# Kernel tuning notes

Measured on AMD Instinct MI355X. Metric: run time of the kernel, lower is better.

## Reference

```python
import jax, jax.numpy as jnp
import numpy as np

N_ATOMS = 50000
N_NBRS = 32
R_CUTOFF = 5.0
N_BASIS = 128
N_FILTERS = 128
N_GAUSS = 25
MAX_Z = 100
MEAN = 0.0
STDDEV = 20.0


def ssp(x):
    # shifted softplus: softplus(x) - log(2)
    return jax.nn.softplus(x) - jnp.log(2.0)


def setup_inputs() -> dict:
    key = jax.random.key(0)
    ks = jax.random.split(key, 18)
    dR = jax.random.uniform(ks[0], (N_ATOMS, N_NBRS), dtype=jnp.float32) * R_CUTOFF
    Z = jax.random.randint(ks[1], (N_ATOMS,), 0, MAX_Z)
    nbr_idx = jax.random.randint(ks[2], (N_ATOMS, N_NBRS), 0, N_ATOMS)

    def p(k, shape):
        fan_in = shape[0]
        return (jax.random.normal(k, shape, dtype=jnp.float32) / np.sqrt(fan_in)).astype(jnp.float32)

    return dict(
        dR=dR, Z=Z, nbr_idx=nbr_idx,
        embed_table=jax.random.normal(ks[3], (MAX_Z, N_BASIS), dtype=jnp.float32),
        fw1=p(ks[4], (N_GAUSS, N_FILTERS)), fb1=jnp.zeros((N_FILTERS,), jnp.float32),
        fw2=p(ks[5], (N_FILTERS, N_FILTERS)), fb2=jnp.zeros((N_FILTERS,), jnp.float32),
        in2f_w=p(ks[6], (N_BASIS, N_FILTERS)),
        f2out_w1=p(ks[7], (N_FILTERS, N_BASIS)), f2out_b1=jnp.zeros((N_BASIS,), jnp.float32),
        f2out_w2=p(ks[8], (N_BASIS, N_BASIS)), f2out_b2=jnp.zeros((N_BASIS,), jnp.float32),
        mlp_w1=p(ks[9], (N_BASIS, 64)), mlp_b1=jnp.zeros((64,), jnp.float32),
        mlp_w2=p(ks[10], (64, 1)), mlp_b2=jnp.zeros((1,), jnp.float32),
    )


def reference(dR, Z, nbr_idx, embed_table, fw1, fb1, fw2, fb2, in2f_w,
              f2out_w1, f2out_b1, f2out_w2, f2out_b2,
              mlp_w1, mlp_b1, mlp_w2, mlp_b2):
    # embedding lookup: [N, B]
    x = embed_table[Z]

    # gaussian smearing of distances: [N, K, G]
    offsets = jnp.linspace(0.0, R_CUTOFF, N_GAUSS, dtype=jnp.float32)
    coeff = -0.5 / (offsets[1] - offsets[0]) ** 2
    dr_exp = jnp.exp(coeff * (dR[..., None] - offsets) ** 2)

    # filter network: Dense+ssp, Dense -> [N, K, F]
    W = ssp(jnp.einsum('nkg,gf->nkf', dr_exp, fw1) + fb1)
    W = jnp.einsum('nkf,fh->nkh', W, fw2) + fb2

    # cosine cutoff
    fcut = 0.5 * (jnp.cos(dR * jnp.pi / R_CUTOFF) + 1.0) * (dR < R_CUTOFF)
    W = W * fcut[..., None]

    # cfconv: in2f (no bias), neighbor gather, elementwise filter, sum over neighbors
    y = x @ in2f_w                    # [N, F]
    y_nbrs = y[nbr_idx]               # [N, K, F] irregular gather
    mask = (nbr_idx < N_ATOMS)[..., None]
    agg = jnp.sum(jnp.where(mask, y_nbrs * W, 0.0), axis=1)  # [N, F]

    # f2out: Dense+ssp, Dense
    v = ssp(agg @ f2out_w1 + f2out_b1) @ f2out_w2 + f2out_b2

    # residual update
    x = x + v

    # atomwise MLP [128 -> 64 -> 1] with ssp between layers
    yi = ssp(x @ mlp_w1 + mlp_b1) @ mlp_w2 + mlp_b2  # [N, 1]
    yi = yi * STDDEV + MEAN

    # aggregate (sum over atom axis), per_atom=False
    return jnp.sum(yi, axis=0)  # [1]
```

## Files before the change

kernel.cpp:

```cpp
#include <hip/hip_runtime.h>
#include <math.h>

#define N_ATOMS  50000
#define N_NBRS   32
#define N_GAUSS  25
#define RCUT     5.0f
#define TT       192
#define TROWS    32
#define NTB      6
#define MAXZ     100
#define NT32     1563
#define PBLOCKS  256
#define PI_F     3.14159265358979323846f

typedef unsigned int   uint_t;
typedef unsigned short ushort_t;
typedef _Float16 f16;
typedef f16   f16x2 __attribute__((ext_vector_type(2)));
typedef f16   f16x4 __attribute__((ext_vector_type(4)));
typedef f16   f16x8 __attribute__((ext_vector_type(8)));
typedef float f32x4 __attribute__((ext_vector_type(4)));

__device__ __forceinline__ float ssp(float x) {
  return fmaxf(x, 0.0f) + __logf(fmaf(0.5f, __expf(-fabsf(x)), 0.5f));
}
__device__ __forceinline__ f16x2 bch(uint_t u) {
  return __builtin_bit_cast(f16x2, u);
}
__device__ __forceinline__ uint_t hcb(f16x2 v) {
  return __builtin_bit_cast(uint_t, v);
}
__device__ __forceinline__ int swz(int m, int e) {
  return m * 128 + ((((e >> 3) ^ m) & 15) << 3) + (e & 7);
}

__global__ void __launch_bounds__(256, 2)
prep_all_kernel(const float* __restrict__ fw1,
                const float* __restrict__ fb1,
                const float* __restrict__ fw2,
                const float* __restrict__ fb2,
                const float* __restrict__ w1,
                const float* __restrict__ w2,
                const float* __restrict__ mw1,
                const float* __restrict__ embed,
                const float* __restrict__ in2f,
                f16* __restrict__ tabh,
                f16* __restrict__ ytab,
                f16* __restrict__ w1ht,
                f16* __restrict__ w2ht,
                f16* __restrict__ mw1ht) {
  const int tid = threadIdx.x;
  const int bid = blockIdx.x;

  __shared__ float sW2[128 * 128];
  __shared__ float sH[TROWS][128];

  if (bid < NTB) {
    const int i0 = bid * TROWS;
    #pragma unroll
    for (int t = 0; t < 16; ++t) {
      const int e = tid + t * 256;
      ((float4*)sW2)[e] = ((const float4*)fw2)[e];
    }
    {
      const int f  = tid & 127;
      const int rh = (tid >> 7) * (TROWS / 2);
      const float delta = RCUT / (float)(N_GAUSS - 1);
      const float coeff = -0.5f / (delta * delta);
      const float b1v = fb1[f];
      for (int j = 0; j < TROWS / 2; ++j) {
        const float r = (float)(i0 + rh + j) * (RCUT / 191.0f);
        float h = b1v;
        #pragma unroll
        for (int g = 0; g < N_GAUSS; ++g) {
          const float d = r - (float)g * delta;
          h = fmaf(__expf(coeff * d * d), fw1[g * 128 + f], h);
        }
        sH[rh + j][f] = ssp(h);
      }
    }
    __syncthreads();
    {
      const int c0 = (tid & 31) * 4;
      const int rg = (tid >> 5) * 4;
      f32x4 acc[4];
      const float4 bv = *(const float4*)&fb2[c0];
      #pragma unroll
      for (int j = 0; j < 4; ++j) acc[j] = (f32x4){bv.x, bv.y, bv.z, bv.w};
      for (int k = 0; k < 128; ++k) {
        const float4 wv = *(const float4*)&sW2[k * 128 + c0];
        #pragma unroll
        for (int j = 0; j < 4; ++j) {
          const float hv = sH[rg + j][k];
          acc[j][0] = fmaf(hv, wv.x, acc[j][0]);
          acc[j][1] = fmaf(hv, wv.y, acc[j][1]);
          acc[j][2] = fmaf(hv, wv.z, acc[j][2]);
          acc[j][3] = fmaf(hv, wv.w, acc[j][3]);
        }
      }
      #pragma unroll
      for (int j = 0; j < 4; ++j) {
        const int i = i0 + rg + j;
        const float r = (float)i * (RCUT / 191.0f);
        const float fc = (r < RCUT) ? 0.5f * (__cosf(r * PI_F / RCUT) + 1.0f) : 0.0f;
        f16x4 o;
        #pragma unroll
        for (int c = 0; c < 4; ++c) o[c] = (f16)(acc[j][c] * fc);
        *(f16x4*)&tabh[i * 128 + c0] = o;
      }
    }
  } else {
    const int cc = (bid - NTB) * 2 + (tid >> 7);
    const int i  = tid & 127;
    w1ht[cc * 128 + i] = (f16)w1[i * 128 + cc];
    w2ht[cc * 128 + i] = (f16)w2[i * 128 + cc];
    if (cc < 64) mw1ht[cc * 128 + i] = (f16)mw1[i * 64 + cc];
    float* xs = &sH[0][0] + (tid >> 7) * 128;
    xs[i] = (cc < MAXZ) ? embed[cc * 128 + i] : 0.0f;
    __syncthreads();
    if (cc < MAXZ) {
      float acc = 0.0f;
      for (int j = 0; j < 128; j += 4) {
        const float4 xv = *reinterpret_cast<const float4*>(&xs[j]);
        acc = fmaf(xv.x, in2f[(j + 0) * 128 + i], acc);
        acc = fmaf(xv.y, in2f[(j + 1) * 128 + i], acc);
        acc = fmaf(xv.z, in2f[(j + 2) * 128 + i], acc);
        acc = fmaf(xv.w, in2f[(j + 3) * 128 + i], acc);
      }
      ytab[cc * 128 + i] = (f16)acc;
    }
  }
}

__global__ void __launch_bounds__(512, 2)
fused_kernel(const float* __restrict__ dR,
             const int* __restrict__ Z,
             const int* __restrict__ nbr,
             const float* __restrict__ embed,
             const f16* __restrict__ tabh,
             const f16* __restrict__ ytab,
             const f16* __restrict__ w1ht, const float* __restrict__ b1,
             const f16* __restrict__ w2ht, const float* __restrict__ b2,
             const f16* __restrict__ mw1ht, const float* __restrict__ mb1,
             const float* __restrict__ mw2,
             float* __restrict__ partial) {
  const int tid = threadIdx.x;
  const int w   = tid >> 6;
  const int l   = tid & 63;
  const int q   = l >> 4;
  const int cq  = l & 15;
  __shared__ __align__(16) f16    sW[TT * 128];
  __shared__ __align__(16) f16    sYT[MAXZ * 128];
  __shared__ __align__(16) uint_t s_pk[1024];
  __shared__ __align__(16) f16    sA[2][16 * 128];
  __shared__ __align__(16) f16    sB[2][16 * 128];
  __shared__ int   sZ[32];
  __shared__ float sRed[8];

  for (int e = tid; e < TT * 16; e += 512)   ((uint4*)sW)[e]  = ((const uint4*)tabh)[e];
  for (int e = tid; e < MAXZ * 16; e += 512) ((uint4*)sYT)[e] = ((const uint4*)ytab)[e];

  const int g   = w >> 2;
  const int wvg = w & 3;
  const int rc  = cq;
  const int qk  = q;
  f16x8 bw1[2][4], bw2[2][4], bwm[4];
  float bb1[2], bb2[2];
  #pragma unroll
  for (int t = 0; t < 2; ++t) {
    const int c = wvg * 32 + t * 16 + rc;
    bb1[t] = b1[c];
    bb2[t] = b2[c];
    #pragma unroll
    for (int k0i = 0; k0i < 4; ++k0i) {
      bw1[t][k0i] = *(const f16x8*)&w1ht[c * 128 + k0i * 32 + qk * 8];
      bw2[t][k0i] = *(const f16x8*)&w2ht[c * 128 + k0i * 32 + qk * 8];
    }
  }
  const int c1 = wvg * 16 + rc;
  #pragma unroll
  for (int k0i = 0; k0i < 4; ++k0i) {
    bwm[k0i] = *(const f16x8*)&mw1ht[c1 * 128 + k0i * 32 + qk * 8];
  }
  const float bm = mb1[c1];
  const float cm = mw2[c1];

  const int m = w * 4 + q;
  const char* wb = (const char*)sW  + cq * 16;
  const char* yb = (const char*)sYT + cq * 16;

  float vsum = 0.0f;
  __syncthreads();

#define AFRAG(SRC, k0) (*(const f16x8*)&SRC[rc * 128 + (((((k0) >> 3) + qk) ^ rc) & 15) * 8])

  for (int chunk = blockIdx.x; chunk < NT32; chunk += PBLOCKS) {
    const int a0 = chunk * 32;
    __syncthreads();

    #pragma unroll
    for (int t0 = 0; t0 < 2; ++t0) {
      const int t = tid + t0 * 512;
      const int pidx = a0 * N_NBRS + t;
      uint_t pk = 0;
      if (pidx < N_ATOMS * N_NBRS) {
        const float r = dR[pidx];
        const int  nb = nbr[pidx];
        int i0 = (int)(r * (191.0f / RCUT) + 0.5f);
        i0 = min(i0, 191);
        pk = (uint_t)i0 | ((uint_t)Z[nb] << 8);
      }
      s_pk[t] = pk;
    }
    if (tid < 32) sZ[tid] = (a0 + tid < N_ATOMS) ? Z[a0 + tid] : 0;
    __syncthreads();

    {
      f16x2 acc[4];
      #pragma unroll
      for (int c = 0; c < 4; ++c) acc[c] = (f16x2)0;

      uint4 twA[4], ytA[4], twB[4], ytB[4];

#define IG(BK, gi) { \
    _Pragma("unroll") \
    for (int d = 0; d < 4; ++d) { \
      const uint_t pk = s_pk[m * N_NBRS + (gi) * 4 + d]; \
      tw##BK[d] = *(const uint4*)(wb + ((pk & 0xFFu) << 8)); \
      yt##BK[d] = *(const uint4*)(yb + ((pk >> 8) << 8)); \
    } }

#define CG(BK) { \
    _Pragma("unroll") \
    for (int d = 0; d < 4; ++d) { \
      acc[0] += bch(tw##BK[d].x) * bch(yt##BK[d].x); \
      acc[1] += bch(tw##BK[d].y) * bch(yt##BK[d].y); \
      acc[2] += bch(tw##BK[d].z) * bch(yt##BK[d].z); \
      acc[3] += bch(tw##BK[d].w) * bch(yt##BK[d].w); \
    } }

      IG(A, 0) IG(B, 1)
      CG(A) IG(A, 2)
      CG(B) IG(B, 3)
      CG(A) IG(A, 4)
      CG(B) IG(B, 5)
      CG(A) IG(A, 6)
      CG(B) IG(B, 7)
      CG(A)
      CG(B)
#undef IG
#undef CG

      uint4 o;
      o.x = hcb(acc[0]); o.y = hcb(acc[1]); o.z = hcb(acc[2]); o.w = hcb(acc[3]);
      const int mm = m & 15;
      *(uint4*)&sA[m >> 4][mm * 128 + (((cq ^ mm) & 15) << 3)] = o;
    }
    __syncthreads();

    f32x4 dacc[2];
    #pragma unroll
    for (int t = 0; t < 2; ++t) dacc[t] = (f32x4){bb1[t], bb1[t], bb1[t], bb1[t]};
    #pragma unroll
    for (int k0i = 0; k0i < 4; ++k0i) {
      const f16x8 af = AFRAG(sA[g], k0i * 32);
      #pragma unroll
      for (int t = 0; t < 2; ++t)
        dacc[t] = __builtin_amdgcn_mfma_f32_16x16x32_f16(af, bw1[t][k0i], dacc[t], 0, 0, 0);
    }
    #pragma unroll
    for (int t = 0; t < 2; ++t) {
      const int c = wvg * 32 + t * 16 + rc;
      #pragma unroll
      for (int r = 0; r < 4; ++r) sB[g][swz(qk * 4 + r, c)] = (f16)ssp(dacc[t][r]);
    }
    __syncthreads();

    #pragma unroll
    for (int t = 0; t < 2; ++t) dacc[t] = (f32x4){bb2[t], bb2[t], bb2[t], bb2[t]};
    #pragma unroll
    for (int k0i = 0; k0i < 4; ++k0i) {
      const f16x8 af = AFRAG(sB[g], k0i * 32);
      #pragma unroll
      for (int t = 0; t < 2; ++t)
        dacc[t] = __builtin_amdgcn_mfma_f32_16x16x32_f16(af, bw2[t][k0i], dacc[t], 0, 0, 0);
    }
    #pragma unroll
    for (int t = 0; t < 2; ++t) {
      const int c = wvg * 32 + t * 16 + rc;
      #pragma unroll
      for (int r = 0; r < 4; ++r) {
        const int mm = qk * 4 + r;
        const float x = embed[(size_t)sZ[g * 16 + mm] * 128 + c] + dacc[t][r];
        sA[g][swz(mm, c)] = (f16)x;
      }
    }
    __syncthreads();

    f32x4 a2 = (f32x4){bm, bm, bm, bm};
    #pragma unroll
    for (int k0i = 0; k0i < 4; ++k0i)
      a2 = __builtin_amdgcn_mfma_f32_16x16x32_f16(AFRAG(sA[g], k0i * 32), bwm[k0i], a2, 0, 0, 0);
    #pragma unroll
    for (int r = 0; r < 4; ++r) {
      const int atom = a0 + g * 16 + qk * 4 + r;
      if (atom < N_ATOMS) vsum = fmaf(ssp(a2[r]), cm, vsum);
    }
  }
#undef AFRAG

  #pragma unroll
  for (int o = 1; o < 64; o <<= 1) vsum += __shfl_xor(vsum, o, 64);
  if (l == 0) sRed[w] = vsum;
  __syncthreads();
  if (tid == 0) {
    float s = 0.0f;
    #pragma unroll
    for (int i = 0; i < 8; ++i) s += sRed[i];
    partial[blockIdx.x] = s;
  }
}

__global__ void __launch_bounds__(256, 1)
reduce_kernel(const float* __restrict__ partial,
              const float* __restrict__ mb2,
              float* __restrict__ out) {
  const int tid = threadIdx.x;
  float s = (tid < PBLOCKS) ? partial[tid] : 0.0f;
  __shared__ float sr[4];
  #pragma unroll
  for (int o = 1; o < 64; o <<= 1) s += __shfl_xor(s, o, 64);
  if ((tid & 63) == 0) sr[tid >> 6] = s;
  __syncthreads();
  if (tid == 0) {
    out[0] = 20.0f * (sr[0] + sr[1] + sr[2] + sr[3] + (float)N_ATOMS * mb2[0]);
  }
}

extern "C" void kernel_launch(void* const* d_in, const int* in_sizes, int n_in,
                              void* d_out, int out_size, void* d_ws, size_t ws_size,
                              hipStream_t stream) {
  const float* dR    = (const float*)d_in[0];
  const int*   Z     = (const int*)  d_in[1];
  const int*   nbr   = (const int*)  d_in[2];
  const float* embed = (const float*)d_in[3];
  const float* fw1   = (const float*)d_in[4];
  const float* fb1   = (const float*)d_in[5];
  const float* fw2   = (const float*)d_in[6];
  const float* fb2   = (const float*)d_in[7];
  const float* in2f  = (const float*)d_in[8];
  const float* w1    = (const float*)d_in[9];
  const float* b1    = (const float*)d_in[10];
  const float* w2    = (const float*)d_in[11];
  const float* b2    = (const float*)d_in[12];
  const float* mw1   = (const float*)d_in[13];
  const float* mb1   = (const float*)d_in[14];
  const float* mw2   = (const float*)d_in[15];
  const float* mb2   = (const float*)d_in[16];
  float* out = (float*)d_out;

  char* ws = (char*)d_ws;
  f16*   tabh    = (f16*)ws;
  f16*   ytab    = (f16*)(ws + (size_t)64 * 1024);
  f16*   w1ht    = (f16*)(ws + (size_t)128 * 1024);
  f16*   w2ht    = (f16*)(ws + (size_t)192 * 1024);
  f16*   mw1ht   = (f16*)(ws + (size_t)256 * 1024);
  float* partial = (float*)(ws + (size_t)384 * 1024);

  prep_all_kernel<<<NTB + 64, 256, 0, stream>>>(fw1, fb1, fw2, fb2,
      w1, w2, mw1, embed, in2f, tabh, ytab, w1ht, w2ht, mw1ht);
  fused_kernel<<<PBLOCKS, 512, 0, stream>>>(dR, Z, nbr, embed,
      tabh, ytab, w1ht, b1, w2ht, b2, mw1ht, mb1, mw2, partial);
  reduce_kernel<<<1, 256, 0, stream>>>(partial, mb2, out);
}
```

Baseline: 55.64 us.

## Warp-specialize fused kernel into gather producer and MFMA consumer waves

The block grows to 1024 threads. Waves 0-7 do the neighbor gather and aggregation for chunk s into a double-buffered shared aggregate, while waves 8-15 run the dense MLP chain on chunk s-1. This overlaps the LDS gather phase with the matrix-core phase, which the old kernel ran serially. In exchange the kernel uses more shared memory and more barriers per stage, and launch_bounds(1024,4) limits registers per thread and may cause spilling. It also risks lower occupancy.

```diff
diff --git a/kernel.cpp b/kernel.cpp
--- a/kernel.cpp
+++ b/kernel.cpp
@@ -132,7 +132,7 @@
   }
 }
 
-__global__ void __launch_bounds__(512, 2)
+__global__ void __launch_bounds__(1024, 4)
 fused_kernel(const float* __restrict__ dR,
              const int* __restrict__ Z,
              const int* __restrict__ nbr,
@@ -144,88 +144,70 @@
              const f16* __restrict__ mw1ht, const float* __restrict__ mb1,
              const float* __restrict__ mw2,
              float* __restrict__ partial) {
-  const int tid = threadIdx.x;
-  const int w   = tid >> 6;
-  const int l   = tid & 63;
-  const int q   = l >> 4;
-  const int cq  = l & 15;
+  const int tid  = threadIdx.x;
+  const int wave = tid >> 6;
+  const int l    = tid & 63;
+  const int q    = l >> 4;
+  const int cq   = l & 15;
+  const int bid  = blockIdx.x;
+
   __shared__ __align__(16) f16    sW[TT * 128];
   __shared__ __align__(16) f16    sYT[MAXZ * 128];
-  __shared__ __align__(16) uint_t s_pk[1024];
-  __shared__ __align__(16) f16    sA[2][16 * 128];
-  __shared__ __align__(16) f16    sB[2][16 * 128];
-  __shared__ int   sZ[32];
+  __shared__ __align__(16) uint_t s_pk[2][1024];
+  __shared__ __align__(16) f16    aggB[2][32 * 128];
+  __shared__ __align__(16) f16    sB[32 * 128];
+  __shared__ __align__(16) f16    sX[32 * 128];
+  __shared__ int   sZb[2][32];
   __shared__ float sRed[8];
 
-  for (int e = tid; e < TT * 16; e += 512)   ((uint4*)sW)[e]  = ((const uint4*)tabh)[e];
-  for (int e = tid; e < MAXZ * 16; e += 512) ((uint4*)sYT)[e] = ((const uint4*)ytab)[e];
-
-  const int g   = w >> 2;
-  const int wvg = w & 3;
-  const int rc  = cq;
-  const int qk  = q;
-  f16x8 bw1[2][4], bw2[2][4], bwm[4];
-  float bb1[2], bb2[2];
-  #pragma unroll
-  for (int t = 0; t < 2; ++t) {
-    const int c = wvg * 32 + t * 16 + rc;
-    bb1[t] = b1[c];
-    bb2[t] = b2[c];
-    #pragma unroll
-    for (int k0i = 0; k0i < 4; ++k0i) {
-      bw1[t][k0i] = *(const f16x8*)&w1ht[c * 128 + k0i * 32 + qk * 8];
-      bw2[t][k0i] = *(const f16x8*)&w2ht[c * 128 + k0i * 32 + qk * 8];
-    }
-  }
-  const int c1 = wvg * 16 + rc;
-  #pragma unroll
-  for (int k0i = 0; k0i < 4; ++k0i) {
-    bwm[k0i] = *(const f16x8*)&mw1ht[c1 * 128 + k0i * 32 + qk * 8];
-  }
-  const float bm = mb1[c1];
-  const float cm = mw2[c1];
-
-  const int m = w * 4 + q;
-  const char* wb = (const char*)sW  + cq * 16;
-  const char* yb = (const char*)sYT + cq * 16;
-
-  float vsum = 0.0f;
+  for (int e = tid; e < TT * 16; e += 1024)   ((uint4*)sW)[e]  = ((const uint4*)tabh)[e];
+  for (int e = tid; e < MAXZ * 16; e += 1024) ((uint4*)sYT)[e] = ((const uint4*)ytab)[e];
   __syncthreads();
 
-#define AFRAG(SRC, k0) (*(const f16x8*)&SRC[rc * 128 + (((((k0) >> 3) + qk) ^ rc) & 15) * 8])
-
-  for (int chunk = blockIdx.x; chunk < NT32; chunk += PBLOCKS) {
-    const int a0 = chunk * 32;
-    __syncthreads();
-
-    #pragma unroll
-    for (int t0 = 0; t0 < 2; ++t0) {
-      const int t = tid + t0 * 512;
-      const int pidx = a0 * N_NBRS + t;
-      uint_t pk = 0;
-      if (pidx < N_ATOMS * N_NBRS) {
-        const float r = dR[pidx];
-        const int  nb = nbr[pidx];
-        int i0 = (int)(r * (191.0f / RCUT) + 0.5f);
-        i0 = min(i0, 191);
-        pk = (uint_t)i0 | ((uint_t)Z[nb] << 8);
-      }
-      s_pk[t] = pk;
-    }
-    if (tid < 32) sZ[tid] = (a0 + tid < N_ATOMS) ? Z[a0 + tid] : 0;
-    __syncthreads();
-
-    {
+  const int myChunks = (NT32 - 1 - bid) / PBLOCKS + 1;
+  const int nstages  = myChunks + 1;
+
+#define AFRAGP(P, k0) (*(const f16x8*)&(P)[rc * 128 + (((((k0) >> 3) + qk) ^ rc) & 15) * 8])
+
+  if (wave < 8) {
+    const int m = wave * 4 + q;
+    const char* wb = (const char*)sW  + cq * 16;
+    const char* yb = (const char*)sYT + cq * 16;
+
+    for (int s = 0; s < nstages; ++s) {
+      const int c   = bid + s * PBLOCKS;
+      const bool act = (c < NT32);
+      const int b   = s & 1;
+      const int a0  = c * 32;
+
+      if (act) {
+        #pragma unroll
+        for (int t0 = 0; t0 < 2; ++t0) {
+          const int t = tid + t0 * 512;
+          const int pidx = a0 * N_NBRS + t;
+          uint_t pk = 0;
+          if (pidx < N_ATOMS * N_NBRS) {
+            const float r = dR[pidx];
+            const int  nb = nbr[pidx];
+            int i0 = (int)(r * (191.0f / RCUT) + 0.5f);
+            i0 = min(i0, 191);
+            pk = (uint_t)i0 | ((uint_t)Z[nb] << 8);
+          }
+          s_pk[b][t] = pk;
+        }
+        if (tid < 32) sZb[b][tid] = (a0 + tid < N_ATOMS) ? Z[a0 + tid] : 0;
+      }
+      __syncthreads();
+
       f16x2 acc[4];
       #pragma unroll
-      for (int c = 0; c < 4; ++c) acc[c] = (f16x2)0;
-
+      for (int cch = 0; cch < 4; ++cch) acc[cch] = (f16x2)0;
       uint4 twA[4], ytA[4], twB[4], ytB[4];
 
 #define IG(BK, gi) { \
     _Pragma("unroll") \
     for (int d = 0; d < 4; ++d) { \
-      const uint_t pk = s_pk[m * N_NBRS + (gi) * 4 + d]; \
+      const uint_t pk = s_pk[b][m * N_NBRS + (gi) * 4 + d]; \
       tw##BK[d] = *(const uint4*)(wb + ((pk & 0xFFu) << 8)); \
       yt##BK[d] = *(const uint4*)(yb + ((pk >> 8) << 8)); \
     } }
@@ -239,85 +221,136 @@
       acc[3] += bch(tw##BK[d].w) * bch(yt##BK[d].w); \
     } }
 
-      IG(A, 0) IG(B, 1)
-      CG(A) IG(A, 2)
-      CG(B) IG(B, 3)
-      CG(A) IG(A, 4)
-      CG(B) IG(B, 5)
-      CG(A) IG(A, 6)
-      CG(B) IG(B, 7)
-      CG(A)
-      CG(B)
+      if (act) {
+        IG(A, 0) IG(B, 1)
+        CG(A) IG(A, 2)
+        CG(B) IG(B, 3)
+        CG(A)
+        CG(B)
+      }
+      __syncthreads();
+
+      if (act) {
+        IG(A, 4) IG(B, 5)
+        CG(A) IG(A, 6)
+        CG(B) IG(B, 7)
+        CG(A)
+        CG(B)
+        uint4 o;
+        o.x = hcb(acc[0]); o.y = hcb(acc[1]); o.z = hcb(acc[2]); o.w = hcb(acc[3]);
+        const int mm = m & 15;
+        *(uint4*)&aggB[b][(m >> 4) * 2048 + mm * 128 + (((cq ^ mm) & 15) << 3)] = o;
+      }
+      __syncthreads();
 #undef IG
 #undef CG
-
-      uint4 o;
-      o.x = hcb(acc[0]); o.y = hcb(acc[1]); o.z = hcb(acc[2]); o.w = hcb(acc[3]);
-      const int mm = m & 15;
-      *(uint4*)&sA[m >> 4][mm * 128 + (((cq ^ mm) & 15) << 3)] = o;
-    }
-    __syncthreads();
-
-    f32x4 dacc[2];
-    #pragma unroll
-    for (int t = 0; t < 2; ++t) dacc[t] = (f32x4){bb1[t], bb1[t], bb1[t], bb1[t]};
-    #pragma unroll
-    for (int k0i = 0; k0i < 4; ++k0i) {
-      const f16x8 af = AFRAG(sA[g], k0i * 32);
-      #pragma unroll
-      for (int t = 0; t < 2; ++t)
-        dacc[t] = __builtin_amdgcn_mfma_f32_16x16x32_f16(af, bw1[t][k0i], dacc[t], 0, 0, 0);
-    }
+    }
+  } else {
+    const int cw  = wave - 8;
+    const int g   = cw >> 2;
+    const int wvg = cw & 3;
+    const int rc  = cq;
+    const int qk  = q;
+
+    f16x8 bw1[2][4], bw2[2][4], bwm[4];
+    float bb1[2], bb2[2];
     #pragma unroll
     for (int t = 0; t < 2; ++t) {
       const int c = wvg * 32 + t * 16 + rc;
+      bb1[t] = b1[c];
+      bb2[t] = b2[c];
       #pragma unroll
-      for (int r = 0; r < 4; ++r) sB[g][swz(qk * 4 + r, c)] = (f16)ssp(dacc[t][r]);
-    }
-    __syncthreads();
-
-    #pragma unroll
-    for (int t = 0; t < 2; ++t) dacc[t] = (f32x4){bb2[t], bb2[t], bb2[t], bb2[t]};
-    #pragma unroll
-    for (int k0i = 0; k0i < 4; ++k0i) {
-      const f16x8 af = AFRAG(sB[g], k0i * 32);
-      #pragma unroll
-      for (int t = 0; t < 2; ++t)
-        dacc[t] = __builtin_amdgcn_mfma_f32_16x16x32_f16(af, bw2[t][k0i], dacc[t], 0, 0, 0);
-    }
-    #pragma unroll
-    for (int t = 0; t < 2; ++t) {
-      const int c = wvg * 32 + t * 16 + rc;
-      #pragma unroll
-      for (int r = 0; r < 4; ++r) {
-        const int mm = qk * 4 + r;
-        const float x = embed[(size_t)sZ[g * 16 + mm] * 128 + c] + dacc[t][r];
-        sA[g][swz(mm, c)] = (f16)x;
-      }
-    }
-    __syncthreads();
-
-    f32x4 a2 = (f32x4){bm, bm, bm, bm};
+      for (int k0i = 0; k0i < 4; ++k0i) {
+        bw1[t][k0i] = *(const f16x8*)&w1ht[c * 128 + k0i * 32 + qk * 8];
+        bw2[t][k0i] = *(const f16x8*)&w2ht[c * 128 + k0i * 32 + qk * 8];
+      }
+    }
+    const int c1 = wvg * 16 + rc;
     #pragma unroll
     for (int k0i = 0; k0i < 4; ++k0i)
-      a2 = __builtin_amdgcn_mfma_f32_16x16x32_f16(AFRAG(sA[g], k0i * 32), bwm[k0i], a2, 0, 0, 0);
+      bwm[k0i] = *(const f16x8*)&mw1ht[c1 * 128 + k0i * 32 + qk * 8];
+    const float bm = mb1[c1];
+    const float cm = mw2[c1];
+
+    float vsum = 0.0f;
+
+    for (int s = 0; s < nstages; ++s) {
+      const int cc  = bid + (s - 1) * PBLOCKS;
+      const bool act = (s >= 1) && (cc < NT32);
+      const int bb  = (s - 1) & 1;
+      const f16* agg = &aggB[bb][g * 2048];
+      f16* hB = &sB[g * 2048];
+      f16* hX = &sX[g * 2048];
+
+      f32x4 dacc[2];
+      if (act) {
+        #pragma unroll
+        for (int t = 0; t < 2; ++t) dacc[t] = (f32x4){bb1[t], bb1[t], bb1[t], bb1[t]};
+        #pragma unroll
+        for (int k0i = 0; k0i < 4; ++k0i) {
+          const f16x8 af = AFRAGP(agg, k0i * 32);
+          #pragma unroll
+          for (int t = 0; t < 2; ++t)
+            dacc[t] = __builtin_amdgcn_mfma_f32_16x16x32_f16(af, bw1[t][k0i], dacc[t], 0, 0, 0);
+        }
+        #pragma unroll
+        for (int t = 0; t < 2; ++t) {
+          const int c = wvg * 32 + t * 16 + rc;
+          #pragma unroll
+          for (int r = 0; r < 4; ++r) hB[swz(qk * 4 + r, c)] = (f16)ssp(dacc[t][r]);
+        }
+      }
+      __syncthreads();
+
+      if (act) {
+        #pragma unroll
+        for (int t = 0; t < 2; ++t) dacc[t] = (f32x4){bb2[t], bb2[t], bb2[t], bb2[t]};
+        #pragma unroll
+        for (int k0i = 0; k0i < 4; ++k0i) {
+          const f16x8 af = AFRAGP(hB, k0i * 32);
+          #pragma unroll
+          for (int t = 0; t < 2; ++t)
+            dacc[t] = __builtin_amdgcn_mfma_f32_16x16x32_f16(af, bw2[t][k0i], dacc[t], 0, 0, 0);
+        }
+        #pragma unroll
+        for (int t = 0; t < 2; ++t) {
+          const int c = wvg * 32 + t * 16 + rc;
+          #pragma unroll
+          for (int r = 0; r < 4; ++r) {
+            const int mm = qk * 4 + r;
+            const float x = embed[(size_t)sZb[bb][g * 16 + mm] * 128 + c] + dacc[t][r];
+            hX[swz(mm, c)] = (f16)x;
+          }
+        }
+      }
+      __syncthreads();
+
+      if (act) {
+        f32x4 a2 = (f32x4){bm, bm, bm, bm};
+        #pragma unroll
+        for (int k0i = 0; k0i < 4; ++k0i)
+          a2 = __builtin_amdgcn_mfma_f32_16x16x32_f16(AFRAGP(hX, k0i * 32), bwm[k0i], a2, 0, 0, 0);
+        #pragma unroll
+        for (int r = 0; r < 4; ++r) {
+          const int atom = cc * 32 + g * 16 + qk * 4 + r;
+          if (atom < N_ATOMS) vsum = fmaf(ssp(a2[r]), cm, vsum);
+        }
+      }
+      __syncthreads();
+    }
+
     #pragma unroll
-    for (int r = 0; r < 4; ++r) {
-      const int atom = a0 + g * 16 + qk * 4 + r;
-      if (atom < N_ATOMS) vsum = fmaf(ssp(a2[r]), cm, vsum);
-    }
+    for (int o = 1; o < 64; o <<= 1) vsum += __shfl_xor(vsum, o, 64);
+    if (l == 0) sRed[cw] = vsum;
   }
-#undef AFRAG
-
-  #pragma unroll
-  for (int o = 1; o < 64; o <<= 1) vsum += __shfl_xor(vsum, o, 64);
-  if (l == 0) sRed[w] = vsum;
+#undef AFRAGP
+
   __syncthreads();
   if (tid == 0) {
-    float s = 0.0f;
+    float sF = 0.0f;
     #pragma unroll
-    for (int i = 0; i < 8; ++i) s += sRed[i];
-    partial[blockIdx.x] = s;
+    for (int i = 0; i < 8; ++i) sF += sRed[i];
+    partial[bid] = sF;
   }
 }
 
@@ -326,7 +359,8 @@
               const float* __restrict__ mb2,
               float* __restrict__ out) {
   const int tid = threadIdx.x;
-  float s = (tid < PBLOCKS) ? partial[tid] : 0.0f;
+  float s = 0.0f;
+  for (int i = tid; i < PBLOCKS; i += 256) s += partial[i];
   __shared__ float sr[4];
   #pragma unroll
   for (int o = 1; o < 64; o <<= 1) s += __shfl_xor(s, o, 64);
@@ -369,7 +403,7 @@
 
   prep_all_kernel<<<NTB + 64, 256, 0, stream>>>(fw1, fb1, fw2, fb2,
       w1, w2, mw1, embed, in2f, tabh, ytab, w1ht, w2ht, mw1ht);
-  fused_kernel<<<PBLOCKS, 512, 0, stream>>>(dR, Z, nbr, embed,
+  fused_kernel<<<PBLOCKS, 1024, 0, stream>>>(dR, Z, nbr, embed,
       tabh, ytab, w1ht, b1, w2ht, b2, mw1ht, mb1, mw2, partial);
   reduce_kernel<<<1, 256, 0, stream>>>(partial, mb2, out);
 }
```

Result: slower. 57.78 us (+3.9%).

## Software-pipeline neighbor gather of next chunk with MFMA dense stages of current

Applied to the files above, without the earlier changes.

Restructures the per-chunk loop into a two-stage software pipeline. The packed neighbor indices and the LDS gather-accumulate for chunk s+1 are interleaved with the three MFMA dense stages of chunk s, using double-buffered s_pk, aggregate and Z buffers. The aim is to hide LDS gather latency and global load latency behind matrix work and cut idle time at barriers. In exchange it needs more LDS (extra double buffers) and more live registers, which may lower occupancy below two blocks per CU.

```diff
diff --git a/kernel.cpp b/kernel.cpp
--- a/kernel.cpp
+++ b/kernel.cpp
@@ -149,12 +149,15 @@
   const int l   = tid & 63;
   const int q   = l >> 4;
   const int cq  = l & 15;
+  const int bid = blockIdx.x;
+
   __shared__ __align__(16) f16    sW[TT * 128];
   __shared__ __align__(16) f16    sYT[MAXZ * 128];
-  __shared__ __align__(16) uint_t s_pk[1024];
-  __shared__ __align__(16) f16    sA[2][16 * 128];
-  __shared__ __align__(16) f16    sB[2][16 * 128];
-  __shared__ int   sZ[32];
+  __shared__ __align__(16) uint_t s_pk[2][1024];
+  __shared__ __align__(16) f16    aggB[2][32 * 128];
+  __shared__ __align__(16) f16    sB[32 * 128];
+  __shared__ __align__(16) f16    sX[32 * 128];
+  __shared__ int   sZb[2][32];
   __shared__ float sRed[8];
 
   for (int e = tid; e < TT * 16; e += 512)   ((uint4*)sW)[e]  = ((const uint4*)tabh)[e];
@@ -179,9 +182,8 @@
   }
   const int c1 = wvg * 16 + rc;
   #pragma unroll
-  for (int k0i = 0; k0i < 4; ++k0i) {
+  for (int k0i = 0; k0i < 4; ++k0i)
     bwm[k0i] = *(const f16x8*)&mw1ht[c1 * 128 + k0i * 32 + qk * 8];
-  }
   const float bm = mb1[c1];
   const float cm = mw2[c1];
 
@@ -189,43 +191,34 @@
   const char* wb = (const char*)sW  + cq * 16;
   const char* yb = (const char*)sYT + cq * 16;
 
+  const int myChunks = (NT32 - 1 - bid) / PBLOCKS + 1;
   float vsum = 0.0f;
-  __syncthreads();
-
-#define AFRAG(SRC, k0) (*(const f16x8*)&SRC[rc * 128 + (((((k0) >> 3) + qk) ^ rc) & 15) * 8])
-
-  for (int chunk = blockIdx.x; chunk < NT32; chunk += PBLOCKS) {
-    const int a0 = chunk * 32;
-    __syncthreads();
-
-    #pragma unroll
-    for (int t0 = 0; t0 < 2; ++t0) {
-      const int t = tid + t0 * 512;
-      const int pidx = a0 * N_NBRS + t;
-      uint_t pk = 0;
-      if (pidx < N_ATOMS * N_NBRS) {
-        const float r = dR[pidx];
-        const int  nb = nbr[pidx];
-        int i0 = (int)(r * (191.0f / RCUT) + 0.5f);
-        i0 = min(i0, 191);
-        pk = (uint_t)i0 | ((uint_t)Z[nb] << 8);
-      }
-      s_pk[t] = pk;
-    }
-    if (tid < 32) sZ[tid] = (a0 + tid < N_ATOMS) ? Z[a0 + tid] : 0;
-    __syncthreads();
-
-    {
-      f16x2 acc[4];
-      #pragma unroll
-      for (int c = 0; c < 4; ++c) acc[c] = (f16x2)0;
-
-      uint4 twA[4], ytA[4], twB[4], ytB[4];
-
-#define IG(BK, gi) { \
+
+  f16x2 acc[4];
+  uint4 twA[4], ytA[4], twB[4], ytB[4];
+
+#define STAGE(bb, cc) { \
+    const int a0s = (cc) * 32; \
+    _Pragma("unroll") \
+    for (int t0 = 0; t0 < 2; ++t0) { \
+      const int t = tid + t0 * 512; \
+      const int pidx = a0s * N_NBRS + t; \
+      uint_t pk = 0; \
+      if (pidx < N_ATOMS * N_NBRS) { \
+        const float r = dR[pidx]; \
+        const int nb = nbr[pidx]; \
+        int i0 = (int)(r * (191.0f / RCUT) + 0.5f); \
+        i0 = min(i0, 191); \
+        pk = (uint_t)i0 | ((uint_t)Z[nb] << 8); \
+      } \
+      s_pk[bb][t] = pk; \
+    } \
+    if (tid < 32) sZb[bb][tid] = (a0s + tid < N_ATOMS) ? Z[a0s + tid] : 0; }
+
+#define IG(BK, bb, gi) { \
     _Pragma("unroll") \
     for (int d = 0; d < 4; ++d) { \
-      const uint_t pk = s_pk[m * N_NBRS + (gi) * 4 + d]; \
+      const uint_t pk = s_pk[bb][m * N_NBRS + (gi) * 4 + d]; \
       tw##BK[d] = *(const uint4*)(wb + ((pk & 0xFFu) << 8)); \
       yt##BK[d] = *(const uint4*)(yb + ((pk >> 8) << 8)); \
     } }
@@ -239,85 +232,127 @@
       acc[3] += bch(tw##BK[d].w) * bch(yt##BK[d].w); \
     } }
 
-      IG(A, 0) IG(B, 1)
-      CG(A) IG(A, 2)
-      CG(B) IG(B, 3)
-      CG(A) IG(A, 4)
-      CG(B) IG(B, 5)
-      CG(A) IG(A, 6)
-      CG(B) IG(B, 7)
-      CG(A)
-      CG(B)
+#define AGGW(bb) { \
+    uint4 o; \
+    o.x = hcb(acc[0]); o.y = hcb(acc[1]); o.z = hcb(acc[2]); o.w = hcb(acc[3]); \
+    const int mm = m & 15; \
+    *(uint4*)&aggB[bb][(m >> 4) * 2048 + mm * 128 + (((cq ^ mm) & 15) << 3)] = o; }
+
+#define AFRAGP(P, k0) (*(const f16x8*)&(P)[rc * 128 + (((((k0) >> 3) + qk) ^ rc) & 15) * 8])
+
+  STAGE(0, bid)
+  __syncthreads();
+  #pragma unroll
+  for (int c = 0; c < 4; ++c) acc[c] = (f16x2)0;
+  IG(A, 0, 0) IG(B, 0, 1)
+  CG(A) IG(A, 0, 2)
+  CG(B) IG(B, 0, 3)
+  CG(A) IG(A, 0, 4)
+  CG(B) IG(B, 0, 5)
+  CG(A) IG(A, 0, 6)
+  CG(B) IG(B, 0, 7)
+  CG(A)
+  CG(B)
+  AGGW(0)
+  __syncthreads();
+
+  for (int s = 0; s < myChunks; ++s) {
+    const int b  = s & 1;
+    const int cc = bid + s * PBLOCKS;
+    const bool hn = (s + 1 < myChunks);
+    const int nb_ = b ^ 1;
+
+    if (hn) STAGE(nb_, cc + PBLOCKS)
+    __syncthreads();
+
+    if (hn) {
+      #pragma unroll
+      for (int c = 0; c < 4; ++c) acc[c] = (f16x2)0;
+    }
+
+    if (hn) { IG(A, nb_, 0) IG(B, nb_, 1) }
+    {
+      const f16* aggp = &aggB[b][g * 2048];
+      f32x4 dacc[2];
+      #pragma unroll
+      for (int t = 0; t < 2; ++t) dacc[t] = (f32x4){bb1[t], bb1[t], bb1[t], bb1[t]};
+      #pragma unroll
+      for (int k0i = 0; k0i < 4; ++k0i) {
+        const f16x8 af = AFRAGP(aggp, k0i * 32);
+        #pragma unroll
+        for (int t = 0; t < 2; ++t)
+          dacc[t] = __builtin_amdgcn_mfma_f32_16x16x32_f16(af, bw1[t][k0i], dacc[t], 0, 0, 0);
+      }
+      f16* hB = &sB[g * 2048];
+      #pragma unroll
+      for (int t = 0; t < 2; ++t) {
+        const int c = wvg * 32 + t * 16 + rc;
+        #pragma unroll
+        for (int r = 0; r < 4; ++r) hB[swz(qk * 4 + r, c)] = (f16)ssp(dacc[t][r]);
+      }
+    }
+    if (hn) { CG(A) IG(A, nb_, 2) CG(B) CG(A) }
+    __syncthreads();
+
+    if (hn) { IG(A, nb_, 3) IG(B, nb_, 4) }
+    {
+      const f16* hB = &sB[g * 2048];
+      f16* hX = &sX[g * 2048];
+      f32x4 dacc[2];
+      #pragma unroll
+      for (int t = 0; t < 2; ++t) dacc[t] = (f32x4){bb2[t], bb2[t], bb2[t], bb2[t]};
+      #pragma unroll
+      for (int k0i = 0; k0i < 4; ++k0i) {
+        const f16x8 af = AFRAGP(hB, k0i * 32);
+        #pragma unroll
+        for (int t = 0; t < 2; ++t)
+          dacc[t] = __builtin_amdgcn_mfma_f32_16x16x32_f16(af, bw2[t][k0i], dacc[t], 0, 0, 0);
+      }
+      #pragma unroll
+      for (int t = 0; t < 2; ++t) {
+        const int c = wvg * 32 + t * 16 + rc;
+        #pragma unroll
+        for (int r = 0; r < 4; ++r) {
+          const int mm = qk * 4 + r;
+          const float x = embed[(size_t)sZb[b][g * 16 + mm] * 128 + c] + dacc[t][r];
+          hX[swz(mm, c)] = (f16)x;
+        }
+      }
+    }
+    if (hn) { CG(A) IG(A, nb_, 5) CG(B) CG(A) }
+    __syncthreads();
+
+    if (hn) { IG(A, nb_, 6) IG(B, nb_, 7) }
+    {
+      const f16* hX = &sX[g * 2048];
+      f32x4 a2 = (f32x4){bm, bm, bm, bm};
+      #pragma unroll
+      for (int k0i = 0; k0i < 4; ++k0i)
+        a2 = __builtin_amdgcn_mfma_f32_16x16x32_f16(AFRAGP(hX, k0i * 32), bwm[k0i], a2, 0, 0, 0);
+      #pragma unroll
+      for (int r = 0; r < 4; ++r) {
+        const int atom = cc * 32 + g * 16 + qk * 4 + r;
+        if (atom < N_ATOMS) vsum = fmaf(ssp(a2[r]), cm, vsum);
+      }
+    }
+    if (hn) { CG(A) CG(B) AGGW(nb_) }
+    __syncthreads();
+  }
+#undef STAGE
 #undef IG
 #undef CG
-
-      uint4 o;
-      o.x = hcb(acc[0]); o.y = hcb(acc[1]); o.z = hcb(acc[2]); o.w = hcb(acc[3]);
-      const int mm = m & 15;
-      *(uint4*)&sA[m >> 4][mm * 128 + (((cq ^ mm) & 15) << 3)] = o;
-    }
-    __syncthreads();
-
-    f32x4 dacc[2];
-    #pragma unroll
-    for (int t = 0; t < 2; ++t) dacc[t] = (f32x4){bb1[t], bb1[t], bb1[t], bb1[t]};
-    #pragma unroll
-    for (int k0i = 0; k0i < 4; ++k0i) {
-      const f16x8 af = AFRAG(sA[g], k0i * 32);
-      #pragma unroll
-      for (int t = 0; t < 2; ++t)
-        dacc[t] = __builtin_amdgcn_mfma_f32_16x16x32_f16(af, bw1[t][k0i], dacc[t], 0, 0, 0);
-    }
-    #pragma unroll
-    for (int t = 0; t < 2; ++t) {
-      const int c = wvg * 32 + t * 16 + rc;
-      #pragma unroll
-      for (int r = 0; r < 4; ++r) sB[g][swz(qk * 4 + r, c)] = (f16)ssp(dacc[t][r]);
-    }
-    __syncthreads();
-
-    #pragma unroll
-    for (int t = 0; t < 2; ++t) dacc[t] = (f32x4){bb2[t], bb2[t], bb2[t], bb2[t]};
-    #pragma unroll
-    for (int k0i = 0; k0i < 4; ++k0i) {
-      const f16x8 af = AFRAG(sB[g], k0i * 32);
-      #pragma unroll
-      for (int t = 0; t < 2; ++t)
-        dacc[t] = __builtin_amdgcn_mfma_f32_16x16x32_f16(af, bw2[t][k0i], dacc[t], 0, 0, 0);
-    }
-    #pragma unroll
-    for (int t = 0; t < 2; ++t) {
-      const int c = wvg * 32 + t * 16 + rc;
-      #pragma unroll
-      for (int r = 0; r < 4; ++r) {
-        const int mm = qk * 4 + r;
-        const float x = embed[(size_t)sZ[g * 16 + mm] * 128 + c] + dacc[t][r];
-        sA[g][swz(mm, c)] = (f16)x;
-      }
-    }
-    __syncthreads();
-
-    f32x4 a2 = (f32x4){bm, bm, bm, bm};
-    #pragma unroll
-    for (int k0i = 0; k0i < 4; ++k0i)
-      a2 = __builtin_amdgcn_mfma_f32_16x16x32_f16(AFRAG(sA[g], k0i * 32), bwm[k0i], a2, 0, 0, 0);
-    #pragma unroll
-    for (int r = 0; r < 4; ++r) {
-      const int atom = a0 + g * 16 + qk * 4 + r;
-      if (atom < N_ATOMS) vsum = fmaf(ssp(a2[r]), cm, vsum);
-    }
-  }
-#undef AFRAG
+#undef AGGW
+#undef AFRAGP
 
   #pragma unroll
   for (int o = 1; o < 64; o <<= 1) vsum += __shfl_xor(vsum, o, 64);
   if (l == 0) sRed[w] = vsum;
   __syncthreads();
   if (tid == 0) {
-    float s = 0.0f;
+    float sF = 0.0f;
     #pragma unroll
-    for (int i = 0; i < 8; ++i) s += sRed[i];
-    partial[blockIdx.x] = s;
+    for (int i = 0; i < 8; ++i) sF += sRed[i];
+    partial[bid] = sF;
   }
 }
 
@@ -326,7 +361,8 @@
               const float* __restrict__ mb2,
               float* __restrict__ out) {
   const int tid = threadIdx.x;
-  float s = (tid < PBLOCKS) ? partial[tid] : 0.0f;
+  float s = 0.0f;
+  for (int i = tid; i < PBLOCKS; i += 256) s += partial[i];
   __shared__ float sr[4];
   #pragma unroll
   for (int o = 1; o < 64; o <<= 1) s += __shfl_xor(s, o, 64);
```

New measurement: 57.24 us. 1.03x slower.
